# Kernel tuning notes

Hardware: AMD Instinct MI355X
Metric: run time of the kernel (lower is better)

The kernel has to match this reference:

```python
import jax, jax.numpy as jnp
import numpy as np

TEMPERATURE = 0.5
EPS = 1e-12  # F.normalize eps


def setup_inputs() -> dict:
    key = jax.random.key(0)
    z = jax.random.normal(key, (2048, 8, 256), dtype=jnp.float32)
    return {"z": z}


def reference(z):
    B, D = z.shape[0], z.shape[1]
    z = z.reshape(B, D, -1)  # [B, D, F]
    # F.normalize along features
    norm = jnp.linalg.norm(z, axis=-1, keepdims=True)
    zn = z / jnp.maximum(norm, EPS)

    # Positive term: per sample b, sim among D views -> [B, D, D], off-diagonal sum
    sim_pos = jnp.exp(jnp.einsum('bdf,bef->bde', zn, zn) / TEMPERATURE)
    eye_d = jnp.eye(D, dtype=bool)
    pos = jnp.sum(jnp.where(eye_d[None], 0.0, sim_pos), axis=(1, 2))  # [B]

    # Negative term: per view d, sim among B samples -> [D, B, B], row-wise off-diag mean, summed over views
    sim_neg = jnp.exp(jnp.einsum('bdf,cdf->dbc', zn, zn) / TEMPERATURE)
    eye_b = jnp.eye(B, dtype=bool)
    neg = jnp.sum(jnp.where(eye_b[None], 0.0, sim_neg), axis=-1) / (B - 1)  # [D, B]
    neg = jnp.sum(neg, axis=0)  # [B]

    logits = pos / (pos + neg)  # [B]
    # torch CrossEntropyLoss(reduction='sum') with 1-D input [C] and float target ones(C):
    # loss = -sum_c target_c * log_softmax(logits)_c = -sum(log_softmax(logits))
    error = -jnp.sum(jax.nn.log_softmax(logits))
    return error / B
```

## Files before the change

kernel.cpp:

```cpp
#include <hip/hip_runtime.h>
#include <hip/hip_bf16.h>

#define B_N 2048
#define D_V 8
#define F_D 256
#define TILE 128
#define BC 64
#define LSTR 264

typedef __attribute__((ext_vector_type(8))) short short8;
typedef __attribute__((ext_vector_type(4))) float floatx4;

__device__ inline unsigned short f2bf(float f) {
    __hip_bfloat16 h = __float2bfloat16(f);
    return *reinterpret_cast<unsigned short*>(&h);
}

__device__ inline float wave_reduce_sum(float v) {
    #pragma unroll
    for (int off = 1; off < 64; off <<= 1)
        v += __shfl_xor(v, off, 64);
    return v;
}

__global__ void norm_kernel(const float* __restrict__ z,
                            unsigned short* __restrict__ zn,
                            float* __restrict__ ns8) {
    int gid = blockIdx.x * blockDim.x + threadIdx.x;
    if (gid < D_V * B_N) ns8[gid] = 0.0f;
    int wave = gid >> 6;
    int lane = threadIdx.x & 63;
    const float4* zp = (const float4*)(z + (size_t)wave * F_D);
    float4 v = zp[lane];
    float ss = v.x * v.x + v.y * v.y + v.z * v.z + v.w * v.w;
    ss = wave_reduce_sum(ss);
    float inv = 1.0f / fmaxf(sqrtf(ss), 1e-12f);
    int b = wave >> 3, d = wave & 7;
    unsigned short* op = zn + (size_t)d * (B_N * F_D) + (size_t)b * F_D + lane * 4;
    ushort4 o;
    o.x = f2bf(v.x * inv);
    o.y = f2bf(v.y * inv);
    o.z = f2bf(v.z * inv);
    o.w = f2bf(v.w * inv);
    *(ushort4*)op = o;
}

__global__ void pos_kernel(const unsigned short* __restrict__ zn,
                           float* __restrict__ pos) {
    int gw = (blockIdx.x * blockDim.x + threadIdx.x) >> 6;
    int lane = threadIdx.x & 63;
    int q = lane >> 4, li = lane & 15;
    int s0 = gw * 2;
    int b = s0 + (li >> 3), d = li & 7;
    const unsigned short* rowp = zn + (size_t)d * (B_N * F_D) + (size_t)b * F_D;
    short8 a[8];
    #pragma unroll
    for (int kk = 0; kk < 8; kk++)
        a[kk] = *(const short8*)(rowp + kk * 32 + q * 8);
    floatx4 acc = {0.f, 0.f, 0.f, 0.f};
    #pragma unroll
    for (int kk = 0; kk < 8; kk++)
        acc = __builtin_amdgcn_mfma_f32_16x16x32_bf16(a[kk], a[kk], acc, 0, 0, 0);
    float p0 = 0.f, p1 = 0.f;
    #pragma unroll
    for (int r = 0; r < 4; r++) {
        int row = q * 4 + r, col = li;
        bool same_sample = (row >> 3) == (col >> 3);
        if (same_sample && row != col) {
            float e = __expf(2.0f * acc[r]);
            if (row < 8) p0 += e; else p1 += e;
        }
    }
    p0 = wave_reduce_sum(p0);
    p1 = wave_reduce_sum(p1);
    if (lane == 0) { pos[s0] = p0; pos[s0 + 1] = p1; }
}

__global__ __launch_bounds__(128, 2)
void neg_kernel(const unsigned short* __restrict__ zn,
                float* __restrict__ ns8) {
    __shared__ __align__(16) unsigned short Bs[BC * LSTR];
    __shared__ float csred[2][TILE];
    const int d = blockIdx.y;
    int trem = blockIdx.x;
    int i = 0;
    while (trem >= 16 - i) { trem -= 16 - i; ++i; }
    const int j = i + trem;
    const bool diag = (i == j);
    const unsigned short* Z = zn + (size_t)d * (B_N * F_D);
    int tid = threadIdx.x, w = tid >> 6, lane = tid & 63;
    int q = lane >> 4, li = lane & 15;
    int r0 = i * TILE + w * 64;

    short8 a[4][8];
    #pragma unroll
    for (int s = 0; s < 4; s++)
        #pragma unroll
        for (int kk = 0; kk < 8; kk++)
            a[s][kk] = *(const short8*)(Z + (size_t)(r0 + s * 16 + li) * F_D + kk * 32 + q * 8);

    float rs[4][4];
    #pragma unroll
    for (int s = 0; s < 4; s++)
        #pragma unroll
        for (int r = 0; r < 4; r++) rs[s][r] = 0.f;
    float cacc[2] = {0.f, 0.f};

    for (int stage = 0; stage < 2; ++stage) {
        int c0 = j * TILE + stage * BC;
        __syncthreads();
        #pragma unroll
        for (int it = 0; it < 16; ++it) {
            int idx = it * 128 + tid;
            int row = idx >> 5, kc = idx & 31;
            *(short8*)(&Bs[row * LSTR + kc * 8]) =
                *(const short8*)(Z + (size_t)(c0 + row) * F_D + kc * 8);
        }
        __syncthreads();
        #pragma unroll
        for (int ct = 0; ct < 4; ++ct) {
            short8 bf[8];
            #pragma unroll
            for (int kk = 0; kk < 8; kk++)
                bf[kk] = *(const short8*)(&Bs[(ct * 16 + li) * LSTR + kk * 32 + q * 8]);
            floatx4 acc[4];
            #pragma unroll
            for (int s = 0; s < 4; s++) acc[s] = (floatx4){0.f, 0.f, 0.f, 0.f};
            #pragma unroll
            for (int kk = 0; kk < 8; kk++)
                #pragma unroll
                for (int s = 0; s < 4; s++)
                    acc[s] = __builtin_amdgcn_mfma_f32_16x16x32_bf16(a[s][kk], bf[kk], acc[s], 0, 0, 0);
            int gcol = c0 + ct * 16 + li;
            float csum = 0.f;
            #pragma unroll
            for (int s = 0; s < 4; s++) {
                #pragma unroll
                for (int r = 0; r < 4; r++) {
                    float e = __expf(2.0f * acc[s][r]);
                    int grow = r0 + s * 16 + q * 4 + r;
                    e = (diag && grow == gcol) ? 0.f : e;
                    rs[s][r] += e;
                    csum += e;
                }
            }
            csum += __shfl_xor(csum, 16, 64);
            csum += __shfl_xor(csum, 32, 64);
            if (q == ct) cacc[stage] += csum;
        }
    }

    #pragma unroll
    for (int off = 1; off < 16; off <<= 1)
        #pragma unroll
        for (int s = 0; s < 4; s++)
            #pragma unroll
            for (int r = 0; r < 4; r++)
                rs[s][r] += __shfl_xor(rs[s][r], off, 64);
    if (li == 0) {
        #pragma unroll
        for (int s = 0; s < 4; s++)
            #pragma unroll
            for (int r = 0; r < 4; r++)
                atomicAdd(&ns8[d * B_N + r0 + s * 16 + q * 4 + r], rs[s][r]);
    }

    csred[w][lane] = cacc[0];
    csred[w][64 + lane] = cacc[1];
    __syncthreads();
    if (!diag && tid < TILE) {
        float v = csred[0][tid] + csred[1][tid];
        atomicAdd(&ns8[d * B_N + j * TILE + tid], v);
    }
}

__global__ void final_kernel(const float* __restrict__ pos,
                             const float* __restrict__ ns8,
                             float* __restrict__ out) {
    __shared__ float red[256];
    int t = threadIdx.x;
    float vals[8];
    float lmax = -1e30f;
    #pragma unroll
    for (int i = 0; i < 8; i++) {
        int idx = t * 8 + i;
        float nsum = 0.f;
        #pragma unroll
        for (int d = 0; d < D_V; d++) nsum += ns8[d * B_N + idx];
        float p = pos[idx];
        float n = nsum * (1.0f / (float)(B_N - 1));
        float l = p / (p + n);
        vals[i] = l;
        lmax = fmaxf(lmax, l);
    }
    red[t] = lmax; __syncthreads();
    for (int s = 128; s > 0; s >>= 1) {
        if (t < s) red[t] = fmaxf(red[t], red[t + s]);
        __syncthreads();
    }
    float m = red[0]; __syncthreads();
    float se = 0.f, sl = 0.f;
    #pragma unroll
    for (int i = 0; i < 8; i++) { se += expf(vals[i] - m); sl += vals[i]; }
    red[t] = se; __syncthreads();
    for (int s = 128; s > 0; s >>= 1) {
        if (t < s) red[t] += red[t + s];
        __syncthreads();
    }
    float S = red[0]; __syncthreads();
    red[t] = sl; __syncthreads();
    for (int s = 128; s > 0; s >>= 1) {
        if (t < s) red[t] += red[t + s];
        __syncthreads();
    }
    if (t == 0) out[0] = m + logf(S) - red[0] / (float)B_N;
}

extern "C" void kernel_launch(void* const* d_in, const int* in_sizes, int n_in,
                              void* d_out, int out_size, void* d_ws, size_t ws_size,
                              hipStream_t stream) {
    const float* z = (const float*)d_in[0];
    float* out = (float*)d_out;
    unsigned short* zn = (unsigned short*)d_ws;
    float* ns8 = (float*)((char*)d_ws + (size_t)D_V * B_N * F_D * 2);
    float* pos = ns8 + D_V * B_N;

    norm_kernel<<<dim3(4096), 256, 0, stream>>>(z, zn, ns8);
    pos_kernel<<<dim3(256), 256, 0, stream>>>(zn, pos);
    neg_kernel<<<dim3(136, 8), 128, 0, stream>>>(zn, ns8);
    final_kernel<<<1, 256, 0, stream>>>(pos, ns8, out);
}
```

Measured before the change: 96.22 us.

## Use FP8 scaled MFMA for negative similarity and fuse final reduction via ticket

The normalization kernel now also writes an FP8 (e4m3) copy of the normalized embeddings. The negative-term kernel uses the 16x16x128 f8f6f4 scaled MFMA on these bytes, which halves global and LDS traffic and quarters the MFMA instruction count. The separate final kernel is removed: the last block to finish, chosen by an atomic ticket counter, computes the log-softmax loss. FP8 precision in the exp(2*sim) terms can reduce accuracy.

```diff
diff --git a/kernel.cpp b/kernel.cpp
--- a/kernel.cpp
+++ b/kernel.cpp
@@ -6,10 +6,12 @@
 #define F_D 256
 #define TILE 128
 #define BC 64
-#define LSTR 264
+#define LSTRB 272
+#define NTILES 136
 
 typedef __attribute__((ext_vector_type(8))) short short8;
 typedef __attribute__((ext_vector_type(4))) float floatx4;
+typedef __attribute__((ext_vector_type(8))) int int8v;
 
 __device__ inline unsigned short f2bf(float f) {
     __hip_bfloat16 h = __float2bfloat16(f);
@@ -25,9 +27,12 @@
 
 __global__ void norm_kernel(const float* __restrict__ z,
                             unsigned short* __restrict__ zn,
-                            float* __restrict__ ns8) {
+                            unsigned char* __restrict__ zn8,
+                            float* __restrict__ ns8,
+                            unsigned int* __restrict__ counter) {
     int gid = blockIdx.x * blockDim.x + threadIdx.x;
     if (gid < D_V * B_N) ns8[gid] = 0.0f;
+    if (gid == 0) *counter = 0u;
     int wave = gid >> 6;
     int lane = threadIdx.x & 63;
     const float4* zp = (const float4*)(z + (size_t)wave * F_D);
@@ -35,14 +40,16 @@
     float ss = v.x * v.x + v.y * v.y + v.z * v.z + v.w * v.w;
     ss = wave_reduce_sum(ss);
     float inv = 1.0f / fmaxf(sqrtf(ss), 1e-12f);
+    float x0 = v.x * inv, x1 = v.y * inv, x2 = v.z * inv, x3 = v.w * inv;
     int b = wave >> 3, d = wave & 7;
-    unsigned short* op = zn + (size_t)d * (B_N * F_D) + (size_t)b * F_D + lane * 4;
+    size_t rowoff = (size_t)d * (B_N * F_D) + (size_t)b * F_D;
     ushort4 o;
-    o.x = f2bf(v.x * inv);
-    o.y = f2bf(v.y * inv);
-    o.z = f2bf(v.z * inv);
-    o.w = f2bf(v.w * inv);
-    *(ushort4*)op = o;
+    o.x = f2bf(x0); o.y = f2bf(x1); o.z = f2bf(x2); o.w = f2bf(x3);
+    *(ushort4*)(zn + rowoff + lane * 4) = o;
+    int packed = 0;
+    packed = __builtin_amdgcn_cvt_pk_fp8_f32(x0, x1, packed, false);
+    packed = __builtin_amdgcn_cvt_pk_fp8_f32(x2, x3, packed, true);
+    *(int*)(zn8 + rowoff + lane * 4) = packed;
 }
 
 __global__ void pos_kernel(const unsigned short* __restrict__ zn,
@@ -77,27 +84,38 @@
 }
 
 __global__ __launch_bounds__(128, 2)
-void neg_kernel(const unsigned short* __restrict__ zn,
-                float* __restrict__ ns8) {
-    __shared__ __align__(16) unsigned short Bs[BC * LSTR];
+void neg_kernel(const unsigned char* __restrict__ zn8,
+                const float* __restrict__ pos,
+                float* __restrict__ ns8,
+                unsigned int* __restrict__ counter,
+                float* __restrict__ out) {
+    __shared__ __align__(16) unsigned char Bs[BC * LSTRB];
     __shared__ float csred[2][TILE];
+    __shared__ unsigned int sticket;
     const int d = blockIdx.y;
     int trem = blockIdx.x;
     int i = 0;
     while (trem >= 16 - i) { trem -= 16 - i; ++i; }
     const int j = i + trem;
     const bool diag = (i == j);
-    const unsigned short* Z = zn + (size_t)d * (B_N * F_D);
+    const unsigned char* Z = zn8 + (size_t)d * (B_N * F_D);
     int tid = threadIdx.x, w = tid >> 6, lane = tid & 63;
     int q = lane >> 4, li = lane & 15;
     int r0 = i * TILE + w * 64;
 
-    short8 a[4][8];
-    #pragma unroll
-    for (int s = 0; s < 4; s++)
-        #pragma unroll
-        for (int kk = 0; kk < 8; kk++)
-            a[s][kk] = *(const short8*)(Z + (size_t)(r0 + s * 16 + li) * F_D + kk * 32 + q * 8);
+    int8v a[4][2];
+    #pragma unroll
+    for (int s = 0; s < 4; s++) {
+        #pragma unroll
+        for (int ki = 0; ki < 2; ki++) {
+            const int4* p = (const int4*)(Z + (size_t)(r0 + s * 16 + li) * F_D + ki * 128 + q * 32);
+            int4 lo = p[0], hi = p[1];
+            int8v t;
+            t[0] = lo.x; t[1] = lo.y; t[2] = lo.z; t[3] = lo.w;
+            t[4] = hi.x; t[5] = hi.y; t[6] = hi.z; t[7] = hi.w;
+            a[s][ki] = t;
+        }
+    }
 
     float rs[4][4];
     #pragma unroll
@@ -110,27 +128,32 @@
         int c0 = j * TILE + stage * BC;
         __syncthreads();
         #pragma unroll
-        for (int it = 0; it < 16; ++it) {
+        for (int it = 0; it < 8; ++it) {
             int idx = it * 128 + tid;
-            int row = idx >> 5, kc = idx & 31;
-            *(short8*)(&Bs[row * LSTR + kc * 8]) =
-                *(const short8*)(Z + (size_t)(c0 + row) * F_D + kc * 8);
+            int row = idx >> 4, kc = idx & 15;
+            *(int4*)(&Bs[row * LSTRB + kc * 16]) =
+                *(const int4*)(Z + (size_t)(c0 + row) * F_D + kc * 16);
         }
         __syncthreads();
         #pragma unroll
         for (int ct = 0; ct < 4; ++ct) {
-            short8 bf[8];
-            #pragma unroll
-            for (int kk = 0; kk < 8; kk++)
-                bf[kk] = *(const short8*)(&Bs[(ct * 16 + li) * LSTR + kk * 32 + q * 8]);
             floatx4 acc[4];
             #pragma unroll
             for (int s = 0; s < 4; s++) acc[s] = (floatx4){0.f, 0.f, 0.f, 0.f};
             #pragma unroll
-            for (int kk = 0; kk < 8; kk++)
+            for (int ki = 0; ki < 2; ki++) {
+                const unsigned char* bp = &Bs[(ct * 16 + li) * LSTRB + ki * 128 + q * 32];
+                int4 lo = *(const int4*)bp;
+                int4 hi = *(const int4*)(bp + 16);
+                int8v bv;
+                bv[0] = lo.x; bv[1] = lo.y; bv[2] = lo.z; bv[3] = lo.w;
+                bv[4] = hi.x; bv[5] = hi.y; bv[6] = hi.z; bv[7] = hi.w;
                 #pragma unroll
                 for (int s = 0; s < 4; s++)
-                    acc[s] = __builtin_amdgcn_mfma_f32_16x16x32_bf16(a[s][kk], bf[kk], acc[s], 0, 0, 0);
+                    acc[s] = __builtin_amdgcn_mfma_scale_f32_16x16x128_f8f6f4(
+                        a[s][ki], bv, acc[s], 0, 0,
+                        0, 0x7f7f7f7f, 0, 0x7f7f7f7f);
+            }
             int gcol = c0 + ct * 16 + li;
             float csum = 0.f;
             #pragma unroll
@@ -172,48 +195,48 @@
         float v = csred[0][tid] + csred[1][tid];
         atomicAdd(&ns8[d * B_N + j * TILE + tid], v);
     }
-}
-
-__global__ void final_kernel(const float* __restrict__ pos,
-                             const float* __restrict__ ns8,
-                             float* __restrict__ out) {
-    __shared__ float red[256];
-    int t = threadIdx.x;
-    float vals[8];
-    float lmax = -1e30f;
-    #pragma unroll
-    for (int i = 0; i < 8; i++) {
-        int idx = t * 8 + i;
-        float nsum = 0.f;
-        #pragma unroll
-        for (int d = 0; d < D_V; d++) nsum += ns8[d * B_N + idx];
-        float p = pos[idx];
-        float n = nsum * (1.0f / (float)(B_N - 1));
-        float l = p / (p + n);
-        vals[i] = l;
-        lmax = fmaxf(lmax, l);
-    }
-    red[t] = lmax; __syncthreads();
-    for (int s = 128; s > 0; s >>= 1) {
-        if (t < s) red[t] = fmaxf(red[t], red[t + s]);
-        __syncthreads();
-    }
-    float m = red[0]; __syncthreads();
-    float se = 0.f, sl = 0.f;
-    #pragma unroll
-    for (int i = 0; i < 8; i++) { se += expf(vals[i] - m); sl += vals[i]; }
-    red[t] = se; __syncthreads();
-    for (int s = 128; s > 0; s >>= 1) {
-        if (t < s) red[t] += red[t + s];
-        __syncthreads();
-    }
-    float S = red[0]; __syncthreads();
-    red[t] = sl; __syncthreads();
-    for (int s = 128; s > 0; s >>= 1) {
-        if (t < s) red[t] += red[t + s];
-        __syncthreads();
-    }
-    if (t == 0) out[0] = m + logf(S) - red[0] / (float)B_N;
+
+    __syncthreads();
+    if (tid == 0) { __threadfence(); sticket = atomicAdd(counter, 1u); }
+    __syncthreads();
+    if (sticket == (unsigned)(NTILES * D_V - 1)) {
+        __threadfence();
+        float vals[16];
+        float lmax = -1e30f;
+        #pragma unroll
+        for (int ii = 0; ii < 16; ii++) {
+            int idx = ii * 128 + tid;
+            float nsum = 0.f;
+            #pragma unroll
+            for (int dd = 0; dd < D_V; dd++) nsum += ns8[dd * B_N + idx];
+            float p = pos[idx];
+            float l = p / (p + nsum * (1.0f / (float)(B_N - 1)));
+            vals[ii] = l;
+            lmax = fmaxf(lmax, l);
+        }
+        float* red = &csred[0][0];
+        red[tid] = lmax; __syncthreads();
+        for (int s2 = 64; s2 > 0; s2 >>= 1) {
+            if (tid < s2) red[tid] = fmaxf(red[tid], red[tid + s2]);
+            __syncthreads();
+        }
+        float m = red[0]; __syncthreads();
+        float se = 0.f, sl = 0.f;
+        #pragma unroll
+        for (int ii = 0; ii < 16; ii++) { se += expf(vals[ii] - m); sl += vals[ii]; }
+        red[tid] = se; __syncthreads();
+        for (int s2 = 64; s2 > 0; s2 >>= 1) {
+            if (tid < s2) red[tid] += red[tid + s2];
+            __syncthreads();
+        }
+        float S = red[0]; __syncthreads();
+        red[tid] = sl; __syncthreads();
+        for (int s2 = 64; s2 > 0; s2 >>= 1) {
+            if (tid < s2) red[tid] += red[tid + s2];
+            __syncthreads();
+        }
+        if (tid == 0) out[0] = m + logf(S) - red[0] * (1.0f / (float)B_N);
+    }
 }
 
 extern "C" void kernel_launch(void* const* d_in, const int* in_sizes, int n_in,
@@ -222,11 +245,12 @@
     const float* z = (const float*)d_in[0];
     float* out = (float*)d_out;
     unsigned short* zn = (unsigned short*)d_ws;
-    float* ns8 = (float*)((char*)d_ws + (size_t)D_V * B_N * F_D * 2);
+    unsigned char* zn8 = (unsigned char*)d_ws + (size_t)D_V * B_N * F_D * 2;
+    float* ns8 = (float*)(zn8 + (size_t)D_V * B_N * F_D);
     float* pos = ns8 + D_V * B_N;
-
-    norm_kernel<<<dim3(4096), 256, 0, stream>>>(z, zn, ns8);
+    unsigned int* counter = (unsigned int*)(pos + B_N);
+
+    norm_kernel<<<dim3(4096), 256, 0, stream>>>(z, zn, zn8, ns8, counter);
     pos_kernel<<<dim3(256), 256, 0, stream>>>(zn, pos);
-    neg_kernel<<<dim3(136, 8), 128, 0, stream>>>(zn, ns8);
-    final_kernel<<<1, 256, 0, stream>>>(pos, ns8, out);
-}
+    neg_kernel<<<dim3(NTILES, D_V), 128, 0, stream>>>(zn8, pos, ns8, counter, out);
+}
```

After: 106.1 us. 1.1x slower.

## Use FP8 MFMA for negative similarity matrix and fold temperature into normalization

Applied to the files above, without the earlier changes.

The normalization kernel now also writes an FP8 copy of the normalized vectors, scaled by sqrt(2) so that the 1/temperature factor is folded into the dot product. The negative-term kernel switches from bf16 to fp8 16x16x32 MFMA, which halves operand bytes loaded from global memory and LDS. Its occupancy hint rises from 2 to 4 blocks per CU. FP8 precision may introduce noticeable error in the exp of similarities, and the extra write adds traffic to the norm kernel.

```diff
diff --git a/kernel.cpp b/kernel.cpp
--- a/kernel.cpp
+++ b/kernel.cpp
@@ -6,7 +6,8 @@
 #define F_D 256
 #define TILE 128
 #define BC 64
-#define LSTR 264
+#define LSTRB 272
+#define NTILES 136
 
 typedef __attribute__((ext_vector_type(8))) short short8;
 typedef __attribute__((ext_vector_type(4))) float floatx4;
@@ -25,6 +26,7 @@
 
 __global__ void norm_kernel(const float* __restrict__ z,
                             unsigned short* __restrict__ zn,
+                            unsigned char* __restrict__ zn8,
                             float* __restrict__ ns8) {
     int gid = blockIdx.x * blockDim.x + threadIdx.x;
     if (gid < D_V * B_N) ns8[gid] = 0.0f;
@@ -34,15 +36,17 @@
     float4 v = zp[lane];
     float ss = v.x * v.x + v.y * v.y + v.z * v.z + v.w * v.w;
     ss = wave_reduce_sum(ss);
-    float inv = 1.0f / fmaxf(sqrtf(ss), 1e-12f);
+    float inv = 1.4142135623730951f / fmaxf(sqrtf(ss), 1e-12f);
+    float x0 = v.x * inv, x1 = v.y * inv, x2 = v.z * inv, x3 = v.w * inv;
     int b = wave >> 3, d = wave & 7;
-    unsigned short* op = zn + (size_t)d * (B_N * F_D) + (size_t)b * F_D + lane * 4;
+    size_t rowoff = (size_t)d * (B_N * F_D) + (size_t)b * F_D;
     ushort4 o;
-    o.x = f2bf(v.x * inv);
-    o.y = f2bf(v.y * inv);
-    o.z = f2bf(v.z * inv);
-    o.w = f2bf(v.w * inv);
-    *(ushort4*)op = o;
+    o.x = f2bf(x0); o.y = f2bf(x1); o.z = f2bf(x2); o.w = f2bf(x3);
+    *(ushort4*)(zn + rowoff + lane * 4) = o;
+    int packed = 0;
+    packed = __builtin_amdgcn_cvt_pk_fp8_f32(x0, x1, packed, false);
+    packed = __builtin_amdgcn_cvt_pk_fp8_f32(x2, x3, packed, true);
+    *(int*)(zn8 + rowoff + lane * 4) = packed;
 }
 
 __global__ void pos_kernel(const unsigned short* __restrict__ zn,
@@ -67,7 +71,7 @@
         int row = q * 4 + r, col = li;
         bool same_sample = (row >> 3) == (col >> 3);
         if (same_sample && row != col) {
-            float e = __expf(2.0f * acc[r]);
+            float e = __expf(acc[r]);
             if (row < 8) p0 += e; else p1 += e;
         }
     }
@@ -76,10 +80,10 @@
     if (lane == 0) { pos[s0] = p0; pos[s0 + 1] = p1; }
 }
 
-__global__ __launch_bounds__(128, 2)
-void neg_kernel(const unsigned short* __restrict__ zn,
+__global__ __launch_bounds__(128, 4)
+void neg_kernel(const unsigned char* __restrict__ zn8,
                 float* __restrict__ ns8) {
-    __shared__ __align__(16) unsigned short Bs[BC * LSTR];
+    __shared__ __align__(16) unsigned char Bs[BC * LSTRB];
     __shared__ float csred[2][TILE];
     const int d = blockIdx.y;
     int trem = blockIdx.x;
@@ -87,17 +91,17 @@
     while (trem >= 16 - i) { trem -= 16 - i; ++i; }
     const int j = i + trem;
     const bool diag = (i == j);
-    const unsigned short* Z = zn + (size_t)d * (B_N * F_D);
+    const unsigned char* Z = zn8 + (size_t)d * (B_N * F_D);
     int tid = threadIdx.x, w = tid >> 6, lane = tid & 63;
     int q = lane >> 4, li = lane & 15;
     int r0 = i * TILE + w * 64;
 
-    short8 a[4][8];
+    long a[4][8];
     #pragma unroll
     for (int s = 0; s < 4; s++)
         #pragma unroll
         for (int kk = 0; kk < 8; kk++)
-            a[s][kk] = *(const short8*)(Z + (size_t)(r0 + s * 16 + li) * F_D + kk * 32 + q * 8);
+            a[s][kk] = *(const long*)(Z + (size_t)(r0 + s * 16 + li) * F_D + kk * 32 + q * 8);
 
     float rs[4][4];
     #pragma unroll
@@ -110,19 +114,19 @@
         int c0 = j * TILE + stage * BC;
         __syncthreads();
         #pragma unroll
-        for (int it = 0; it < 16; ++it) {
+        for (int it = 0; it < 8; ++it) {
             int idx = it * 128 + tid;
-            int row = idx >> 5, kc = idx & 31;
-            *(short8*)(&Bs[row * LSTR + kc * 8]) =
-                *(const short8*)(Z + (size_t)(c0 + row) * F_D + kc * 8);
+            int row = idx >> 4, kc = idx & 15;
+            *(int4*)(&Bs[row * LSTRB + kc * 16]) =
+                *(const int4*)(Z + (size_t)(c0 + row) * F_D + kc * 16);
         }
         __syncthreads();
         #pragma unroll
         for (int ct = 0; ct < 4; ++ct) {
-            short8 bf[8];
+            long bf[8];
             #pragma unroll
             for (int kk = 0; kk < 8; kk++)
-                bf[kk] = *(const short8*)(&Bs[(ct * 16 + li) * LSTR + kk * 32 + q * 8]);
+                bf[kk] = *(const long*)(&Bs[(ct * 16 + li) * LSTRB + kk * 32 + q * 8]);
             floatx4 acc[4];
             #pragma unroll
             for (int s = 0; s < 4; s++) acc[s] = (floatx4){0.f, 0.f, 0.f, 0.f};
@@ -130,14 +134,14 @@
             for (int kk = 0; kk < 8; kk++)
                 #pragma unroll
                 for (int s = 0; s < 4; s++)
-                    acc[s] = __builtin_amdgcn_mfma_f32_16x16x32_bf16(a[s][kk], bf[kk], acc[s], 0, 0, 0);
+                    acc[s] = __builtin_amdgcn_mfma_f32_16x16x32_fp8_fp8(a[s][kk], bf[kk], acc[s], 0, 0, 0);
             int gcol = c0 + ct * 16 + li;
             float csum = 0.f;
             #pragma unroll
             for (int s = 0; s < 4; s++) {
                 #pragma unroll
                 for (int r = 0; r < 4; r++) {
-                    float e = __expf(2.0f * acc[s][r]);
+                    float e = __expf(acc[s][r]);
                     int grow = r0 + s * 16 + q * 4 + r;
                     e = (diag && grow == gcol) ? 0.f : e;
                     rs[s][r] += e;
@@ -222,11 +226,12 @@
     const float* z = (const float*)d_in[0];
     float* out = (float*)d_out;
     unsigned short* zn = (unsigned short*)d_ws;
-    float* ns8 = (float*)((char*)d_ws + (size_t)D_V * B_N * F_D * 2);
+    unsigned char* zn8 = (unsigned char*)d_ws + (size_t)D_V * B_N * F_D * 2;
+    float* ns8 = (float*)(zn8 + (size_t)D_V * B_N * F_D);
     float* pos = ns8 + D_V * B_N;
 
-    norm_kernel<<<dim3(4096), 256, 0, stream>>>(z, zn, ns8);
+    norm_kernel<<<dim3(4096), 256, 0, stream>>>(z, zn, zn8, ns8);
     pos_kernel<<<dim3(256), 256, 0, stream>>>(zn, pos);
-    neg_kernel<<<dim3(136, 8), 128, 0, stream>>>(zn, ns8);
+    neg_kernel<<<dim3(NTILES, D_V), 128, 0, stream>>>(zn8, ns8);
     final_kernel<<<1, 256, 0, stream>>>(pos, ns8, out);
 }
```

Measured after the change: 103.8 us. 7.9% more time.
